# Performance work log

Hardware: AMD Instinct MI355X
Metric: run time of the kernel (lower is better)

The kernel has to match this reference:

```python
import jax, jax.numpy as jnp
import numpy as np

B, T, F, H = 512, 1024, 64, 128

def setup_inputs() -> dict:
    key = jax.random.key(0)
    ks = jax.random.split(key, 6)
    x = jax.random.normal(ks[0], (B, T, F), dtype=jnp.float32)
    # Keras LSTM params: kernel [F,4H], recurrent_kernel [H,4H], bias [4H]; gate order i,f,g,o
    W = jax.random.normal(ks[1], (F, 4 * H), dtype=jnp.float32) * (1.0 / np.sqrt(F))
    U = jax.random.normal(ks[2], (H, 4 * H), dtype=jnp.float32) * (1.0 / np.sqrt(H))
    b = jnp.zeros((4 * H,), dtype=jnp.float32)
    Wfc = jax.random.normal(ks[3], (H, 1), dtype=jnp.float32) * (1.0 / np.sqrt(H))
    bfc = jnp.zeros((1,), dtype=jnp.float32)
    return {"x": x, "W": W, "U": U, "b": b, "Wfc": Wfc, "bfc": bfc}

def reference(x, W, U, b, Wfc, bfc):
    # LSTM with recurrent_activation='tanh' (gates i,f,o use tanh, NOT sigmoid);
    # candidate g and cell-output activation are also tanh (Keras defaults).
    batch = x.shape[0]
    h0 = jnp.zeros((batch, H), dtype=x.dtype)
    c0 = jnp.zeros((batch, H), dtype=x.dtype)

    def step(carry, xt):
        h, c = carry
        z = xt @ W + h @ U + b  # [B, 4H]
        i, f, g, o = jnp.split(z, 4, axis=-1)
        i = jnp.tanh(i)
        f = jnp.tanh(f)
        g = jnp.tanh(g)
        o = jnp.tanh(o)
        c_new = f * c + i * g
        h_new = o * jnp.tanh(c_new)
        return (h_new, c_new), None

    xs = jnp.swapaxes(x, 0, 1)  # [T, B, F]
    (h_last, _), _ = jax.lax.scan(step, (h0, c0), xs)
    return h_last @ Wfc + bfc  # [B, 1]
```

## Files before the change

kernel.cpp:

```cpp
#include <hip/hip_runtime.h>

typedef _Float16 h8  __attribute__((ext_vector_type(8)));
typedef _Float16 hh4 __attribute__((ext_vector_type(4)));
typedef float    f4  __attribute__((ext_vector_type(4)));

#define TT 1024
#define FF 64
#define NTH 512
#define GRP 16
#define NGRP (TT / GRP)
#define K2 2.8853900817779268f

#define HSWZ(r, e) ((e) ^ (((r) & 7) << 3))

__device__ __forceinline__ float tanh0(float z) {
  float e = __builtin_amdgcn_exp2f(z * K2);
  return __builtin_fmaf(-2.0f, __builtin_amdgcn_rcpf(e + 1.0f), 1.0f);
}

#define MFMA __builtin_amdgcn_mfma_f32_16x16x32_f16
#define FENCE() __builtin_amdgcn_sched_barrier(0)

__global__ __launch_bounds__(NTH, 2) void lstm_persist(
    const float* __restrict__ X, const float* __restrict__ W,
    const float* __restrict__ U, const float* __restrict__ bias,
    const float* __restrict__ Wfc, const float* __restrict__ bfcp,
    float* __restrict__ out)
{
  const int tid = threadIdx.x;
  const int wv = tid >> 6, ln = tid & 63;
  const int l15 = ln & 15, lg = ln >> 4;
  const int row0 = blockIdx.x * 2;
  const int ncol = wv * 16 + l15;

  __shared__ __align__(16) _Float16 h_s[2][384];
  __shared__ __align__(16) _Float16 x_s[32 * 64];
  __shared__ __align__(16) _Float16 zx_s[32 * 512];
  __shared__ float red[8][2];

  h8 uf[4][4], wf4[4][2];
  f4 bias4[4];
#pragma unroll
  for (int g = 0; g < 4; ++g) {
    const int n = g * 128 + ncol;
#pragma unroll
    for (int f = 0; f < 4; ++f) {
      h8 v;
#pragma unroll
      for (int e = 0; e < 8; ++e) v[e] = (_Float16)U[(32 * f + 8 * lg + e) * 512 + n];
      uf[g][f] = v;
    }
#pragma unroll
    for (int f = 0; f < 2; ++f) {
      h8 v;
#pragma unroll
      for (int e = 0; e < 8; ++e) v[e] = (_Float16)W[(32 * f + 8 * lg + e) * 512 + n];
      wf4[g][f] = v;
    }
    const float bv = bias[n];
    f4 b4 = {bv, bv, bv, bv};
    bias4[g] = b4;
  }
  const float wfc = Wfc[ncol];

  int hofs[4];
#pragma unroll
  for (int f = 0; f < 4; ++f) {
    const int base = 32 * f + 8 * lg;
    hofs[f] = (l15 == 0) ? base : (l15 == 4) ? 128 + base : 0;
  }
  int bxofs[2][2];
#pragma unroll
  for (int mt = 0; mt < 2; ++mt)
#pragma unroll
    for (int f = 0; f < 2; ++f)
      bxofs[mt][f] = HSWZ(l15, (mt * 16 + l15) * 64 + 32 * f + 8 * lg);

  const int zofs  = (lg < 2) ? (lg * 512 + ncol * 4) : 0;
  const int zwofs = ncol * 4;
  const int hwofs = (lg < 2) ? (lg * 128 + ncol) : (256 + ncol);

  const int sm = tid >> 4;
  const int sk = (tid & 15) * 4;
  const int sxofs = HSWZ(sm, sm * 64 + sk);
  const size_t xoff0 = (size_t)(row0 + (sm & 1)) * (TT * FF) + (size_t)(sm >> 1) * FF + sk;

  for (int i = tid; i < 2 * 384; i += NTH) ((_Float16*)h_s)[i] = (_Float16)0.0f;

  f4 xg = *(const f4*)(X + xoff0);
  float cc = 0.f;
  const f4 zq = {0.f, 0.f, 0.f, 0.f};
  hh4 q4cur;
  __syncthreads();

#define STEP(S, CUR, NXT, DOPF) {                                             \
    const _Float16* hb = &h_s[CUR][0];                                        \
    h8 ha0 = *(const h8*)(hb + hofs[0]);                                      \
    h8 ha1 = *(const h8*)(hb + hofs[1]);                                      \
    h8 ha2 = *(const h8*)(hb + hofs[2]);                                      \
    h8 ha3 = *(const h8*)(hb + hofs[3]);                                      \
    f4 a0 = MFMA(ha0, uf[0][0], zq, 0, 0, 0);                                 \
    a0 = MFMA(ha1, uf[0][1], a0, 0, 0, 0);                                    \
    a0 = MFMA(ha2, uf[0][2], a0, 0, 0, 0);                                    \
    a0 = MFMA(ha3, uf[0][3], a0, 0, 0, 0);                                    \
    float ti = tanh0(a0[0] + (float)q4cur[0]);                                \
    FENCE();                                                                  \
    f4 a1 = MFMA(ha0, uf[1][0], zq, 0, 0, 0);                                 \
    a1 = MFMA(ha1, uf[1][1], a1, 0, 0, 0);                                    \
    a1 = MFMA(ha2, uf[1][2], a1, 0, 0, 0);                                    \
    a1 = MFMA(ha3, uf[1][3], a1, 0, 0, 0);                                    \
    float tf = tanh0(a1[0] + (float)q4cur[1]);                                \
    FENCE();                                                                  \
    f4 a2 = MFMA(ha0, uf[2][0], zq, 0, 0, 0);                                 \
    a2 = MFMA(ha1, uf[2][1], a2, 0, 0, 0);                                    \
    a2 = MFMA(ha2, uf[2][2], a2, 0, 0, 0);                                    \
    a2 = MFMA(ha3, uf[2][3], a2, 0, 0, 0);                                    \
    float tg = tanh0(a2[0] + (float)q4cur[2]);                                \
    cc = __builtin_fmaf(tf, cc, ti * tg);                                     \
    FENCE();                                                                  \
    f4 a3 = MFMA(ha0, uf[3][0], zq, 0, 0, 0);                                 \
    a3 = MFMA(ha1, uf[3][1], a3, 0, 0, 0);                                    \
    a3 = MFMA(ha2, uf[3][2], a3, 0, 0, 0);                                    \
    a3 = MFMA(ha3, uf[3][3], a3, 0, 0, 0);                                    \
    float to = tanh0(a3[0] + (float)q4cur[3]);                                \
    float hv = to * tanh0(cc);                                                \
    h_s[NXT][hwofs] = (_Float16)hv;                                           \
    if (DOPF) q4cur = *(const hh4*)(&zx_s[zofs + ((S) + 1) * 1024]);          \
    __syncthreads();                                                          \
  }

#pragma unroll 1
  for (int grp = 0; grp < NGRP; ++grp) {
    {
      hh4 pk;
#pragma unroll
      for (int j = 0; j < 4; ++j) pk[j] = (_Float16)xg[j];
      *(hh4*)(&x_s[sxofs]) = pk;
    }
    __syncthreads();

    h8 xa00 = *(const h8*)(&x_s[bxofs[0][0]]);
    h8 xa01 = *(const h8*)(&x_s[bxofs[0][1]]);
    h8 xa10 = *(const h8*)(&x_s[bxofs[1][0]]);
    h8 xa11 = *(const h8*)(&x_s[bxofs[1][1]]);
    f4 b00 = MFMA(xa00, wf4[0][0], bias4[0], 0, 0, 0);
    f4 b01 = MFMA(xa00, wf4[1][0], bias4[1], 0, 0, 0);
    f4 b02 = MFMA(xa00, wf4[2][0], bias4[2], 0, 0, 0);
    f4 b03 = MFMA(xa00, wf4[3][0], bias4[3], 0, 0, 0);
    b00 = MFMA(xa01, wf4[0][1], b00, 0, 0, 0);
    b01 = MFMA(xa01, wf4[1][1], b01, 0, 0, 0);
    b02 = MFMA(xa01, wf4[2][1], b02, 0, 0, 0);
    b03 = MFMA(xa01, wf4[3][1], b03, 0, 0, 0);
    f4 b10 = MFMA(xa10, wf4[0][0], bias4[0], 0, 0, 0);
    f4 b11 = MFMA(xa10, wf4[1][0], bias4[1], 0, 0, 0);
    f4 b12 = MFMA(xa10, wf4[2][0], bias4[2], 0, 0, 0);
    f4 b13 = MFMA(xa10, wf4[3][0], bias4[3], 0, 0, 0);
    b10 = MFMA(xa11, wf4[0][1], b10, 0, 0, 0);
    b11 = MFMA(xa11, wf4[1][1], b11, 0, 0, 0);
    b12 = MFMA(xa11, wf4[2][1], b12, 0, 0, 0);
    b13 = MFMA(xa11, wf4[3][1], b13, 0, 0, 0);
#pragma unroll
    for (int j = 0; j < 4; ++j) {
      hh4 p0; p0[0] = (_Float16)b00[j]; p0[1] = (_Float16)b01[j];
              p0[2] = (_Float16)b02[j]; p0[3] = (_Float16)b03[j];
      *(hh4*)(&zx_s[(0 * 16 + 4 * lg + j) * 512 + zwofs]) = p0;
      hh4 p1; p1[0] = (_Float16)b10[j]; p1[1] = (_Float16)b11[j];
              p1[2] = (_Float16)b12[j]; p1[3] = (_Float16)b13[j];
      *(hh4*)(&zx_s[(1 * 16 + 4 * lg + j) * 512 + zwofs]) = p1;
    }
    {
      const int t0n = (grp + 1 < NGRP ? grp + 1 : grp) * GRP;
      xg = *(const f4*)(X + xoff0 + (size_t)t0n * FF);
    }
    __syncthreads();
    q4cur = *(const hh4*)(&zx_s[zofs]);

#pragma unroll
    for (int s2 = 0; s2 < 8; ++s2) {
      STEP(2 * s2,     0, 1, 1)
      STEP(2 * s2 + 1, 1, 0, (2 * s2 + 1) != (GRP - 1))
    }
  }
#undef STEP

  float hw0 = (float)h_s[0][ncol];
  float hw1 = (float)h_s[0][128 + ncol];
  float p0 = hw0 * wfc;
  float p1 = hw1 * wfc;
#pragma unroll
  for (int m = 1; m < 16; m <<= 1) {
    p0 += __shfl_xor(p0, m, 16);
    p1 += __shfl_xor(p1, m, 16);
  }
  if (ln == 0) { red[wv][0] = p0; red[wv][1] = p1; }
  __syncthreads();
  if (tid < 2) {
    float y = bfcp[0];
#pragma unroll
    for (int w2 = 0; w2 < 8; ++w2) y += red[w2][tid];
    out[row0 + tid] = y;
  }
}

extern "C" void kernel_launch(void* const* d_in, const int* in_sizes, int n_in,
                              void* d_out, int out_size, void* d_ws, size_t ws_size,
                              hipStream_t stream) {
  const float* x   = (const float*)d_in[0];
  const float* W   = (const float*)d_in[1];
  const float* U   = (const float*)d_in[2];
  const float* b   = (const float*)d_in[3];
  const float* Wfc = (const float*)d_in[4];
  const float* bfc = (const float*)d_in[5];
  float* out = (float*)d_out;
  hipLaunchKernelGGL(lstm_persist, dim3(256), dim3(NTH), 0, stream,
                     x, W, U, b, Wfc, bfc, out);
}
```

Before: 462.3 us.

## Interleave next-group input projection into recurrent steps with double-buffered zx

Instead of stopping every 16 steps to compute the x@W projection for the whole group, the input projection for the next 8-step group is spread across the recurrent steps of the current group. The results go to a double-buffered zx shared array. This removes the per-group serial bubble and its extra barriers from the critical recurrent chain. The cost is extra MFMA and LDS work inside each step, a smaller group size, and more register pressure.

```diff
diff --git a/kernel.cpp b/kernel.cpp
--- a/kernel.cpp
+++ b/kernel.cpp
@@ -7,7 +7,7 @@
 #define TT 1024
 #define FF 64
 #define NTH 512
-#define GRP 16
+#define GRP 8
 #define NGRP (TT / GRP)
 #define K2 2.8853900817779268f
 
@@ -34,8 +34,8 @@
   const int ncol = wv * 16 + l15;
 
   __shared__ __align__(16) _Float16 h_s[2][384];
-  __shared__ __align__(16) _Float16 x_s[32 * 64];
-  __shared__ __align__(16) _Float16 zx_s[32 * 512];
+  __shared__ __align__(16) _Float16 x_s[16 * 64];
+  __shared__ __align__(16) _Float16 zx_s[2][16 * 512];
   __shared__ float red[8][2];
 
   h8 uf[4][4], wf4[4][2];
@@ -69,12 +69,10 @@
     const int base = 32 * f + 8 * lg;
     hofs[f] = (l15 == 0) ? base : (l15 == 4) ? 128 + base : 0;
   }
-  int bxofs[2][2];
-#pragma unroll
-  for (int mt = 0; mt < 2; ++mt)
-#pragma unroll
-    for (int f = 0; f < 2; ++f)
-      bxofs[mt][f] = HSWZ(l15, (mt * 16 + l15) * 64 + 32 * f + 8 * lg);
+  int bxofs[2];
+#pragma unroll
+  for (int f = 0; f < 2; ++f)
+    bxofs[f] = HSWZ(l15, l15 * 64 + 32 * f + 8 * lg);
 
   const int zofs  = (lg < 2) ? (lg * 512 + ncol * 4) : 0;
   const int zwofs = ncol * 4;
@@ -83,103 +81,130 @@
   const int sm = tid >> 4;
   const int sk = (tid & 15) * 4;
   const int sxofs = HSWZ(sm, sm * 64 + sk);
-  const size_t xoff0 = (size_t)(row0 + (sm & 1)) * (TT * FF) + (size_t)(sm >> 1) * FF + sk;
+  const size_t xbase = (size_t)(row0 + (sm & 1)) * (TT * FF) + (size_t)(sm >> 1) * FF + sk;
 
   for (int i = tid; i < 2 * 384; i += NTH) ((_Float16*)h_s)[i] = (_Float16)0.0f;
 
-  f4 xg = *(const f4*)(X + xoff0);
+  f4 xg;
+  h8 xa0, xa1;
+  f4 b0, b1, b2, b3;
+  if (tid < 256) {
+    xg = *(const f4*)(X + xbase);
+    hh4 pk;
+#pragma unroll
+    for (int j = 0; j < 4; ++j) pk[j] = (_Float16)xg[j];
+    *(hh4*)(&x_s[sxofs]) = pk;
+  }
+  __syncthreads();
+  xa0 = *(const h8*)(&x_s[bxofs[0]]);
+  xa1 = *(const h8*)(&x_s[bxofs[1]]);
+  b0 = MFMA(xa0, wf4[0][0], bias4[0], 0, 0, 0);
+  b1 = MFMA(xa0, wf4[1][0], bias4[1], 0, 0, 0);
+  b2 = MFMA(xa0, wf4[2][0], bias4[2], 0, 0, 0);
+  b3 = MFMA(xa0, wf4[3][0], bias4[3], 0, 0, 0);
+  b0 = MFMA(xa1, wf4[0][1], b0, 0, 0, 0);
+  b1 = MFMA(xa1, wf4[1][1], b1, 0, 0, 0);
+  b2 = MFMA(xa1, wf4[2][1], b2, 0, 0, 0);
+  b3 = MFMA(xa1, wf4[3][1], b3, 0, 0, 0);
+#pragma unroll
+  for (int j = 0; j < 4; ++j) {
+    hh4 p; p[0] = (_Float16)b0[j]; p[1] = (_Float16)b1[j];
+           p[2] = (_Float16)b2[j]; p[3] = (_Float16)b3[j];
+    *(hh4*)(&zx_s[0][(4 * lg + j) * 512 + zwofs]) = p;
+  }
+  if (tid < 256) xg = *(const f4*)(X + xbase + (size_t)GRP * FF);
   float cc = 0.f;
   const f4 zq = {0.f, 0.f, 0.f, 0.f};
-  hh4 q4cur;
   __syncthreads();
 
-#define STEP(S, CUR, NXT, DOPF) {                                             \
+#define STEP(S, CUR, NXT) {                                                   \
     const _Float16* hb = &h_s[CUR][0];                                        \
     h8 ha0 = *(const h8*)(hb + hofs[0]);                                      \
     h8 ha1 = *(const h8*)(hb + hofs[1]);                                      \
     h8 ha2 = *(const h8*)(hb + hofs[2]);                                      \
     h8 ha3 = *(const h8*)(hb + hofs[3]);                                      \
+    hh4 q4 = *(const hh4*)(&zx_s[0][0] + zrb + zofs + (S) * 1024);            \
+           \
+    if ((S) == 1) xa0 = *(const h8*)(&x_s[bxofs[0]]);                         \
+    if ((S) == 2) xa1 = *(const h8*)(&x_s[bxofs[1]]);                         \
+    if ((S) == 2) { b0 = MFMA(xa0, wf4[0][0], bias4[0], 0, 0, 0);             \
+                    b1 = MFMA(xa0, wf4[1][0], bias4[1], 0, 0, 0); }           \
+    if ((S) == 3) { b2 = MFMA(xa0, wf4[2][0], bias4[2], 0, 0, 0);             \
+                    b3 = MFMA(xa0, wf4[3][0], bias4[3], 0, 0, 0); }           \
+    if ((S) == 4) { b0 = MFMA(xa1, wf4[0][1], b0, 0, 0, 0);                   \
+                    b1 = MFMA(xa1, wf4[1][1], b1, 0, 0, 0); }                 \
+    if ((S) == 5) { b2 = MFMA(xa1, wf4[2][1], b2, 0, 0, 0);                   \
+                    b3 = MFMA(xa1, wf4[3][1], b3, 0, 0, 0); }                 \
     f4 a0 = MFMA(ha0, uf[0][0], zq, 0, 0, 0);                                 \
     a0 = MFMA(ha1, uf[0][1], a0, 0, 0, 0);                                    \
     a0 = MFMA(ha2, uf[0][2], a0, 0, 0, 0);                                    \
     a0 = MFMA(ha3, uf[0][3], a0, 0, 0, 0);                                    \
-    float ti = tanh0(a0[0] + (float)q4cur[0]);                                \
+    float ti = tanh0(a0[0] + (float)q4[0]);                                   \
     FENCE();                                                                  \
     f4 a1 = MFMA(ha0, uf[1][0], zq, 0, 0, 0);                                 \
     a1 = MFMA(ha1, uf[1][1], a1, 0, 0, 0);                                    \
     a1 = MFMA(ha2, uf[1][2], a1, 0, 0, 0);                                    \
     a1 = MFMA(ha3, uf[1][3], a1, 0, 0, 0);                                    \
-    float tf = tanh0(a1[0] + (float)q4cur[1]);                                \
+    float tf = tanh0(a1[0] + (float)q4[1]);                                   \
     FENCE();                                                                  \
     f4 a2 = MFMA(ha0, uf[2][0], zq, 0, 0, 0);                                 \
     a2 = MFMA(ha1, uf[2][1], a2, 0, 0, 0);                                    \
     a2 = MFMA(ha2, uf[2][2], a2, 0, 0, 0);                                    \
     a2 = MFMA(ha3, uf[2][3], a2, 0, 0, 0);                                    \
-    float tg = tanh0(a2[0] + (float)q4cur[2]);                                \
+    float tg = tanh0(a2[0] + (float)q4[2]);                                   \
     cc = __builtin_fmaf(tf, cc, ti * tg);                                     \
     FENCE();                                                                  \
     f4 a3 = MFMA(ha0, uf[3][0], zq, 0, 0, 0);                                 \
     a3 = MFMA(ha1, uf[3][1], a3, 0, 0, 0);                                    \
     a3 = MFMA(ha2, uf[3][2], a3, 0, 0, 0);                                    \
     a3 = MFMA(ha3, uf[3][3], a3, 0, 0, 0);                                    \
-    float to = tanh0(a3[0] + (float)q4cur[3]);                                \
+    float to = tanh0(a3[0] + (float)q4[3]);                                   \
     float hv = to * tanh0(cc);                                                \
     h_s[NXT][hwofs] = (_Float16)hv;                                           \
-    if (DOPF) q4cur = *(const hh4*)(&zx_s[zofs + ((S) + 1) * 1024]);          \
+        \
+    if ((S) == 0 && tid < 256) {                                              \
+      hh4 pk;                                                                 \
+      _Pragma("unroll")                                                       \
+      for (int j = 0; j < 4; ++j) pk[j] = (_Float16)xg[j];                    \
+      *(hh4*)(&x_s[sxofs]) = pk;                                              \
+    }                                                                         \
+    if ((S) == 3 && tid < 256) {                                              \
+      int t2 = (grp + 2) * GRP; if (t2 >= TT) t2 = TT - GRP;                  \
+      xg = *(const f4*)(X + xbase + (size_t)t2 * FF);                         \
+    }                                                                         \
+    if ((S) == 6) {                                                           \
+      _Float16* zwp = &zx_s[0][0] + zwb + zwofs;                              \
+      _Pragma("unroll")                                                       \
+      for (int j = 0; j < 2; ++j) {                                           \
+        hh4 p; p[0] = (_Float16)b0[j]; p[1] = (_Float16)b1[j];                \
+               p[2] = (_Float16)b2[j]; p[3] = (_Float16)b3[j];                \
+        *(hh4*)(zwp + (4 * lg + j) * 512) = p;                                \
+      }                                                                       \
+    }                                                                         \
+    if ((S) == 7) {                                                           \
+      _Float16* zwp = &zx_s[0][0] + zwb + zwofs;                              \
+      _Pragma("unroll")                                                       \
+      for (int j = 2; j < 4; ++j) {                                           \
+        hh4 p; p[0] = (_Float16)b0[j]; p[1] = (_Float16)b1[j];                \
+               p[2] = (_Float16)b2[j]; p[3] = (_Float16)b3[j];                \
+        *(hh4*)(zwp + (4 * lg + j) * 512) = p;                                \
+      }                                                                       \
+    }                                                                         \
     __syncthreads();                                                          \
   }
 
 #pragma unroll 1
   for (int grp = 0; grp < NGRP; ++grp) {
-    {
-      hh4 pk;
-#pragma unroll
-      for (int j = 0; j < 4; ++j) pk[j] = (_Float16)xg[j];
-      *(hh4*)(&x_s[sxofs]) = pk;
-    }
-    __syncthreads();
-
-    h8 xa00 = *(const h8*)(&x_s[bxofs[0][0]]);
-    h8 xa01 = *(const h8*)(&x_s[bxofs[0][1]]);
-    h8 xa10 = *(const h8*)(&x_s[bxofs[1][0]]);
-    h8 xa11 = *(const h8*)(&x_s[bxofs[1][1]]);
-    f4 b00 = MFMA(xa00, wf4[0][0], bias4[0], 0, 0, 0);
-    f4 b01 = MFMA(xa00, wf4[1][0], bias4[1], 0, 0, 0);
-    f4 b02 = MFMA(xa00, wf4[2][0], bias4[2], 0, 0, 0);
-    f4 b03 = MFMA(xa00, wf4[3][0], bias4[3], 0, 0, 0);
-    b00 = MFMA(xa01, wf4[0][1], b00, 0, 0, 0);
-    b01 = MFMA(xa01, wf4[1][1], b01, 0, 0, 0);
-    b02 = MFMA(xa01, wf4[2][1], b02, 0, 0, 0);
-    b03 = MFMA(xa01, wf4[3][1], b03, 0, 0, 0);
-    f4 b10 = MFMA(xa10, wf4[0][0], bias4[0], 0, 0, 0);
-    f4 b11 = MFMA(xa10, wf4[1][0], bias4[1], 0, 0, 0);
-    f4 b12 = MFMA(xa10, wf4[2][0], bias4[2], 0, 0, 0);
-    f4 b13 = MFMA(xa10, wf4[3][0], bias4[3], 0, 0, 0);
-    b10 = MFMA(xa11, wf4[0][1], b10, 0, 0, 0);
-    b11 = MFMA(xa11, wf4[1][1], b11, 0, 0, 0);
-    b12 = MFMA(xa11, wf4[2][1], b12, 0, 0, 0);
-    b13 = MFMA(xa11, wf4[3][1], b13, 0, 0, 0);
-#pragma unroll
-    for (int j = 0; j < 4; ++j) {
-      hh4 p0; p0[0] = (_Float16)b00[j]; p0[1] = (_Float16)b01[j];
-              p0[2] = (_Float16)b02[j]; p0[3] = (_Float16)b03[j];
-      *(hh4*)(&zx_s[(0 * 16 + 4 * lg + j) * 512 + zwofs]) = p0;
-      hh4 p1; p1[0] = (_Float16)b10[j]; p1[1] = (_Float16)b11[j];
-              p1[2] = (_Float16)b12[j]; p1[3] = (_Float16)b13[j];
-      *(hh4*)(&zx_s[(1 * 16 + 4 * lg + j) * 512 + zwofs]) = p1;
-    }
-    {
-      const int t0n = (grp + 1 < NGRP ? grp + 1 : grp) * GRP;
-      xg = *(const f4*)(X + xoff0 + (size_t)t0n * FF);
-    }
-    __syncthreads();
-    q4cur = *(const hh4*)(&zx_s[zofs]);
-
-#pragma unroll
-    for (int s2 = 0; s2 < 8; ++s2) {
-      STEP(2 * s2,     0, 1, 1)
-      STEP(2 * s2 + 1, 1, 0, (2 * s2 + 1) != (GRP - 1))
-    }
+    const int zrb = (grp & 1) << 13;
+    const int zwb = 8192 - zrb;
+    STEP(0, 0, 1)
+    STEP(1, 1, 0)
+    STEP(2, 0, 1)
+    STEP(3, 1, 0)
+    STEP(4, 0, 1)
+    STEP(5, 1, 0)
+    STEP(6, 0, 1)
+    STEP(7, 1, 0)
   }
 #undef STEP
 
```

New measurement: 465.1 us. Within noise of the previous version (+0.6%).
